# Kernel tuning notes

Measured on AMD Instinct MI355X. Metric: run time of the kernel, lower is better.

The kernel has to match this reference:

```python
import jax, jax.numpy as jnp
import numpy as np
import math

D = 1024      # hidden_size
H = 16        # num_heads
HD = D // H   # head_dim = 64
ROPE = 64     # rope_dim == head_dim (full-head rotation, empty pass-through)
E = 8         # num_experts
F = 2560
BASE = 10000.0
EPS = 1e-5
SPECIALS = jnp.arange(2, 8)  # special_tokens indices {2..7} used as global tokens


def _ln(x, w, b):
    m = x.mean(-1, keepdims=True)
    v = x.var(-1, keepdims=True)  # biased var, matches torch LayerNorm
    return (x - m) / jnp.sqrt(v + EPS) * w + b


def _rope(x, cos, sin):
    # x: [B,H,T,HD]; rotate first ROPE dims via half-split (NOT rotate-half interleave)
    x1, x2 = x[..., : ROPE // 2], x[..., ROPE // 2 : ROPE]
    rot = jnp.concatenate([x1 * cos - x2 * sin, x1 * sin + x2 * cos], axis=-1)
    return jnp.concatenate([rot, x[..., ROPE:]], axis=-1)


def setup_inputs() -> dict:
    key = jax.random.key(0)
    ks = jax.random.split(key, 8)
    B, T = 1, 1024
    g = lambda k, shape, s: (jax.random.normal(k, shape, jnp.float32) * s)
    return {
        "x": g(ks[0], (B, T, D), 1.0),
        "input_ids": jax.random.randint(ks[1], (B, T), 0, 32000),
        "ln1_w": jnp.ones((D,), jnp.float32), "ln1_b": jnp.zeros((D,), jnp.float32),
        "qkv_w": g(ks[2], (D, 3 * D), 0.02), "qkv_b": jnp.zeros((3 * D,), jnp.float32),
        "attn_out_w": g(ks[3], (D, D), 0.02), "attn_out_b": jnp.zeros((D,), jnp.float32),
        "ln2_w": jnp.ones((D,), jnp.float32), "ln2_b": jnp.zeros((D,), jnp.float32),
        "gate_w": g(ks[4], (D, E), 0.02), "gate_b": jnp.zeros((E,), jnp.float32),
        "fc_w": g(ks[5], (E, D, 2 * F), 0.02), "fc_b": jnp.zeros((E, 2 * F), jnp.float32),
        "eout_w": g(ks[6], (E, F, D), 0.02), "eout_b": jnp.zeros((E, D), jnp.float32),
    }


def _block(x, input_ids, ln1_w, ln1_b, qkv_w, qkv_b, attn_out_w, attn_out_b,
           ln2_w, ln2_b, gate_w, gate_b, fc_w, fc_b, eout_w, eout_b):
    B, T, _ = x.shape
    # --- self-attention (pre-norm) ---
    h = _ln(x, ln1_w, ln1_b)
    qkv = h @ qkv_w + qkv_b
    q, k, v = jnp.split(qkv, 3, axis=-1)
    resh = lambda t: t.reshape(B, T, H, HD).transpose(0, 2, 1, 3)  # [B,H,T,HD]
    q, k, v = resh(q), resh(k), resh(v)
    pos = jnp.arange(T, dtype=jnp.float32)
    inv = 1.0 / (BASE ** (jnp.arange(0, ROPE, 2, dtype=jnp.float32) / ROPE))
    fr = pos[:, None] * inv[None, :]            # [T, ROPE/2]
    cos, sin = jnp.cos(fr), jnp.sin(fr)
    q = _rope(q, cos, sin)
    k = _rope(k, cos, sin)
    causal = jnp.tril(jnp.ones((T, T), bool))
    glob = (input_ids[..., None] == SPECIALS).any(-1)            # [B,T]
    allowed = causal[None, None] | glob[:, None, :, None]        # [B,1,T,T]
    logits = jnp.einsum('bhqd,bhkd->bhqk', q, k) / math.sqrt(HD)
    neg = -jnp.finfo(logits.dtype).max
    logits = jnp.where(allowed, logits, neg)
    aw = jax.nn.softmax(logits, axis=-1)
    attn = jnp.einsum('bhqk,bhkd->bhqd', aw, v).transpose(0, 2, 1, 3).reshape(B, T, H * HD)
    x = x + (attn @ attn_out_w + attn_out_b)
    # --- MoE GEGLU FFN (hard top-1 routing) ---
    h2 = _ln(x, ln2_w, ln2_b)
    gp = jax.nn.softmax(h2 @ gate_w + gate_b, axis=-1)           # [B,T,E]
    gw = gp.max(-1)
    gi = gp.argmax(-1)
    xf = h2.reshape(-1, D)
    gif = gi.reshape(-1)
    gwf = gw.reshape(-1)
    N = xf.shape[0]
    outf = jnp.zeros((N, D), x.dtype)
    for e in range(E):  # fixed small expert loop; select by routing mask
        h12 = xf @ fc_w[e] + fc_b[e]
        x1, x2 = h12[:, :F], h12[:, F:]
        y = (x1 * jax.nn.gelu(x2, approximate=False)) @ eout_w[e] + eout_b[e]
        outf = outf + jnp.where((gif == e)[:, None], y, 0.0)
    outf = outf * gwf[:, None]
    sums = jax.ops.segment_sum(gwf, gif, num_segments=E)
    counts = jax.ops.segment_sum(jnp.ones_like(gwf), gif, num_segments=E)
    usage = sums / (counts + 1e-8)
    moe_loss = jnp.sum((usage - 1.0 / E) ** 2)
    return x + outf.reshape(B, T, D), moe_loss


def reference(x, input_ids, ln1_w, ln1_b, qkv_w, qkv_b, attn_out_w, attn_out_b,
              ln2_w, ln2_b, gate_w, gate_b, fc_w, fc_b, eout_w, eout_b):
    return _block(x, input_ids, ln1_w, ln1_b, qkv_w, qkv_b, attn_out_w, attn_out_b,
                  ln2_w, ln2_b, gate_w, gate_b, fc_w, fc_b, eout_w, eout_b)
```

## Files before the change

kernel.cpp:

```cpp
#include <hip/hip_runtime.h>
#include <float.h>
#include <math.h>
#include <stdint.h>

#define T_ 1024
#define D_ 1024
#define H_ 16
#define HD_ 64
#define E_ 8
#define F_ 2560
#define D3_ 3072
#define F2_ 5120

#define WS_H    0u
#define WS_QKV  1048576u
#define WS_ATTN 4194304u
#define WS_X2   5242880u
#define WS_H2   6291456u
#define WS_A    7340032u
#define WS_GW   9961472u
#define WS_GI   9962496u
#define WS_OFFS 9963520u
#define WS_PERM 9963536u

typedef short short8 __attribute__((ext_vector_type(8)));
typedef short short4v __attribute__((ext_vector_type(4)));
typedef __bf16 bf16x8 __attribute__((ext_vector_type(8)));
typedef float floatx4 __attribute__((ext_vector_type(4)));

union FragU { short8 s; bf16x8 b; };

__device__ __forceinline__ short f2bf(float f) {
    union { float f; uint32_t u; } a; a.f = f;
    uint32_t r = a.u + 0x7fffu + ((a.u >> 16) & 1u);
    return (short)(r >> 16);
}

__device__ __forceinline__ void cvt16(const float4& a0, const float4& a1,
                                      const float4& a2, const float4& a3,
                                      short8& c0, short8& c1) {
    c0[0]=f2bf(a0.x); c0[1]=f2bf(a0.y); c0[2]=f2bf(a0.z); c0[3]=f2bf(a0.w);
    c0[4]=f2bf(a1.x); c0[5]=f2bf(a1.y); c0[6]=f2bf(a1.z); c0[7]=f2bf(a1.w);
    c1[0]=f2bf(a2.x); c1[1]=f2bf(a2.y); c1[2]=f2bf(a2.z); c1[3]=f2bf(a2.w);
    c1[4]=f2bf(a3.x); c1[5]=f2bf(a3.y); c1[6]=f2bf(a3.z); c1[7]=f2bf(a3.w);
}

#define GEMM_IDS \
    const int tid  = threadIdx.x;                 \
    const int a_m  = tid >> 1;                    \
    const int a_kh = (tid & 1) * 16;              \
    const int lane = tid & 63, wave = tid >> 6;   \
    const int wm = wave & 1,  wn = wave >> 1;     \
    const int quad = lane >> 4, lm = lane & 15;

__global__ __launch_bounds__(256) void gemm_mfma_full(
    const short* __restrict__ A, int lda,
    const float* __restrict__ B, int ldb,
    const float* __restrict__ bias,
    float* __restrict__ C, int ldc, int K)
{
    __shared__ __align__(16) short As[4*128*8];
    __shared__ __align__(16) short Bs[64*40];
    const int row0 = blockIdx.y * 128, col0 = blockIdx.x * 64;
    GEMM_IDS
    const int b_n = tid >> 2, b_kc = tid & 3;
    floatx4 acc[4][2];
    #pragma unroll
    for (int i=0;i<4;i++)
        #pragma unroll
        for (int j=0;j<2;j++) acc[i][j] = (floatx4){0.f,0.f,0.f,0.f};

    const short* apx = A + (size_t)(row0 + a_m) * lda + a_kh;
    const float* bpx = B + (size_t)(b_kc*8) * ldb + col0 + b_n;
    const int kcA = (tid & 1) * 2;

    short8 sA0, sA1, sB0, sB1;
    float bvA[8], bvB[8];
    sA0 = *(const short8*)(apx);
    sA1 = *(const short8*)(apx + 8);
    sB0 = *(const short8*)(apx + 32);
    sB1 = *(const short8*)(apx + 40);
    #pragma unroll
    for (int j=0;j<8;j++) bvA[j] = bpx[(size_t)j*ldb];
    {
        const float* bp2 = bpx + (size_t)32*ldb;
        #pragma unroll
        for (int j=0;j<8;j++) bvB[j] = bp2[(size_t)j*ldb];
    }

#define GF_STEP(S0,S1,BV,kpre)                                            \
    __syncthreads();                                                      \
    {                                                                     \
        short8 cb;                                                        \
        _Pragma("unroll")                                                 \
        for (int j=0;j<8;j++) cb[j] = f2bf(BV[j]);                        \
        *(short8*)&As[((kcA  )*128 + a_m)*8] = S0;                        \
        *(short8*)&As[((kcA+1)*128 + a_m)*8] = S1;                        \
        *(short8*)&Bs[b_n*40 + b_kc*8] = cb;                              \
    }                                                                     \
    __syncthreads();                                                      \
    if ((kpre) < K) {                                                     \
        S0 = *(const short8*)(apx + (kpre));                              \
        S1 = *(const short8*)(apx + (kpre) + 8);                          \
        const float* bp2 = bpx + (size_t)(kpre) * ldb;                    \
        _Pragma("unroll")                                                 \
        for (int j=0;j<8;j++) BV[j] = bp2[(size_t)j*ldb];                 \
    }                                                                     \
    {                                                                     \
        FragU fa[4], fb[2];                                               \
        _Pragma("unroll")                                                 \
        for (int i=0;i<4;i++) fa[i].s = *(short8*)&As[(quad*128 + wm*64 + i*16 + lm)*8]; \
        _Pragma("unroll")                                                 \
        for (int j=0;j<2;j++) fb[j].s = *(short8*)&Bs[(wn*32 + j*16 + lm)*40 + quad*8];  \
        _Pragma("unroll")                                                 \
        for (int i=0;i<4;i++)                                             \
            _Pragma("unroll")                                             \
            for (int j=0;j<2;j++)                                         \
                acc[i][j] = __builtin_amdgcn_mfma_f32_16x16x32_bf16(fa[i].b, fb[j].b, acc[i][j], 0,0,0); \
    }

    for (int k0 = 0; k0 < K; k0 += 64) {
        GF_STEP(sA0, sA1, bvA, k0 + 64)
        GF_STEP(sB0, sB1, bvB, k0 + 96)
    }
#undef GF_STEP

    #pragma unroll
    for (int i=0;i<4;i++)
        #pragma unroll
        for (int j=0;j<2;j++) {
            int col = col0 + wn*32 + j*16 + lm;
            float bb = bias ? bias[col] : 0.f;
            #pragma unroll
            for (int r=0;r<4;r++) {
                int row = row0 + wm*64 + i*16 + quad*4 + r;
                C[(size_t)row*ldc + col] = acc[i][j][r] + bb;
            }
        }
}

__global__ __launch_bounds__(256) void gemm_mfma_acc(
    const short* __restrict__ A, int lda,
    const float* __restrict__ B, int ldb, long sB,
    const int* __restrict__ offs, const int* __restrict__ perm,
    float* __restrict__ Cacc, int ldc, int K, int nsk)
{
    const int sk = blockIdx.y % nsk;
    const int e  = blockIdx.y / nsk;
    int off = 0, Ne = T_;
    if (offs) { off = offs[e]; Ne = offs[e+1] - off; }
    const int row0 = blockIdx.z * 128;
    if (row0 >= Ne) return;
    const int col0 = blockIdx.x * 64;
    B += (long)e * sB;

    __shared__ __align__(16) short As[4*128*8];
    __shared__ __align__(16) short Bs[64*40];
    __shared__ int toks[128];
    GEMM_IDS
    const int b_n = tid >> 2, b_kc = tid & 3;
    if (tid < 128) {
        int r = row0 + tid;
        toks[tid] = offs ? ((r < Ne) ? perm[off + r] : -1) : r;
    }
    __syncthreads();

    floatx4 acc[4][2];
    #pragma unroll
    for (int i=0;i<4;i++)
        #pragma unroll
        for (int j=0;j<2;j++) acc[i][j] = (floatx4){0.f,0.f,0.f,0.f};

    const int tokA = toks[a_m];
    const short* apx = (tokA >= 0) ? (A + (size_t)tokA * lda + a_kh) : nullptr;
    const float* bpx = B + (size_t)(b_kc*8) * ldb + col0 + b_n;
    const int kcA = (tid & 1) * 2;
    const int Kp = K / nsk;
    const int koff = sk * Kp, kend = koff + Kp;

    short8 sA0 = {0,0,0,0,0,0,0,0}, sA1 = sA0, sB0 = sA0, sB1 = sA0;
    float bvA[8], bvB[8];
    if (apx) {
        sA0 = *(const short8*)(apx + koff);
        sA1 = *(const short8*)(apx + koff + 8);
        sB0 = *(const short8*)(apx + koff + 32);
        sB1 = *(const short8*)(apx + koff + 40);
    }
    {
        const float* bp2 = bpx + (size_t)koff * ldb;
        #pragma unroll
        for (int j=0;j<8;j++) bvA[j] = bp2[(size_t)j*ldb];
        bp2 += (size_t)32 * ldb;
        #pragma unroll
        for (int j=0;j<8;j++) bvB[j] = bp2[(size_t)j*ldb];
    }

#define GA_STEP(S0,S1,BV,kpre)                                            \
    __syncthreads();                                                      \
    {                                                                     \
        short8 cb;                                                        \
        _Pragma("unroll")                                                 \
        for (int j=0;j<8;j++) cb[j] = f2bf(BV[j]);                        \
        *(short8*)&As[((kcA  )*128 + a_m)*8] = S0;                        \
        *(short8*)&As[((kcA+1)*128 + a_m)*8] = S1;                        \
        *(short8*)&Bs[b_n*40 + b_kc*8] = cb;                              \
    }                                                                     \
    __syncthreads();                                                      \
    if ((kpre) < kend) {                                                  \
        if (apx) {                                                        \
            S0 = *(const short8*)(apx + (kpre));                          \
            S1 = *(const short8*)(apx + (kpre) + 8);                      \
        }                                                                 \
        const float* bp2 = bpx + (size_t)(kpre) * ldb;                    \
        _Pragma("unroll")                                                 \
        for (int j=0;j<8;j++) BV[j] = bp2[(size_t)j*ldb];                 \
    }                                                                     \
    {                                                                     \
        FragU fa[4], fb[2];                                               \
        _Pragma("unroll")                                                 \
        for (int i=0;i<4;i++) fa[i].s = *(short8*)&As[(quad*128 + wm*64 + i*16 + lm)*8]; \
        _Pragma("unroll")                                                 \
        for (int j=0;j<2;j++) fb[j].s = *(short8*)&Bs[(wn*32 + j*16 + lm)*40 + quad*8];  \
        _Pragma("unroll")                                                 \
        for (int i=0;i<4;i++)                                             \
            _Pragma("unroll")                                             \
            for (int j=0;j<2;j++)                                         \
                acc[i][j] = __builtin_amdgcn_mfma_f32_16x16x32_bf16(fa[i].b, fb[j].b, acc[i][j], 0,0,0); \
    }

    for (int k0 = koff; k0 < kend; k0 += 64) {
        GA_STEP(sA0, sA1, bvA, k0 + 64)
        GA_STEP(sB0, sB1, bvB, k0 + 96)
    }
#undef GA_STEP

    #pragma unroll
    for (int i=0;i<4;i++)
        #pragma unroll
        for (int j=0;j<2;j++) {
            int col = col0 + wn*32 + j*16 + lm;
            #pragma unroll
            for (int r=0;r<4;r++) {
                int tk = toks[wm*64 + i*16 + quad*4 + r];
                if (tk >= 0) atomicAdd(&Cacc[(size_t)tk*ldc + col], acc[i][j][r]);
            }
        }
}

__global__ __launch_bounds__(256) void moe_fc_mfma(
    const short* __restrict__ h2, const float* __restrict__ fcw,
    const float* __restrict__ fcb, const int* __restrict__ offs,
    const int* __restrict__ perm, short* __restrict__ aout)
{
    const int e = blockIdx.y;
    const int off = offs[e];
    const int Ne = offs[e+1] - off;
    const int row0 = blockIdx.z * 128;
    if (row0 >= Ne) return;
    const int col0 = blockIdx.x * 32;

    __shared__ __align__(16) short As[4*128*8];
    __shared__ __align__(16) short B1s[32*40];
    __shared__ __align__(16) short B2s[32*40];
    __shared__ int toks[128];
    GEMM_IDS
    const int n_l = tid & 31, kg = tid >> 5;
    if (tid < 128) {
        int r = row0 + tid;
        toks[tid] = (r < Ne) ? perm[off + r] : -1;
    }
    __syncthreads();

    floatx4 acc1[4], acc2[4];
    #pragma unroll
    for (int i=0;i<4;i++) {
        acc1[i] = (floatx4){0.f,0.f,0.f,0.f};
        acc2[i] = (floatx4){0.f,0.f,0.f,0.f};
    }

    const float* W = fcw + (size_t)e * D_ * F2_;
    const int tokA = toks[a_m];
    const short* apx = (tokA >= 0) ? (h2 + (size_t)tokA * D_ + a_kh) : nullptr;
    const float* bpx = W + (size_t)(kg*4) * F2_ + col0 + n_l;
    const int kcA = (tid & 1) * 2;

    short8 sA0 = {0,0,0,0,0,0,0,0}, sA1 = sA0, sB0 = sA0, sB1 = sA0;
    float b1A[4], b2A[4], b1B[4], b2B[4];
    if (apx) {
        sA0 = *(const short8*)(apx);
        sA1 = *(const short8*)(apx + 8);
        sB0 = *(const short8*)(apx + 32);
        sB1 = *(const short8*)(apx + 40);
    }
    #pragma unroll
    for (int j=0;j<4;j++) { b1A[j] = bpx[(size_t)j*F2_]; b2A[j] = bpx[(size_t)j*F2_ + F_]; }
    {
        const float* bp2 = bpx + (size_t)32*F2_;
        #pragma unroll
        for (int j=0;j<4;j++) { b1B[j] = bp2[(size_t)j*F2_]; b2B[j] = bp2[(size_t)j*F2_ + F_]; }
    }

#define MF_STEP(S0,S1,BV1,BV2,kpre)                                       \
    __syncthreads();                                                      \
    {                                                                     \
        short4v cb1, cb2;                                                 \
        _Pragma("unroll")                                                 \
        for (int j=0;j<4;j++) { cb1[j] = f2bf(BV1[j]); cb2[j] = f2bf(BV2[j]); } \
        *(short8*)&As[((kcA  )*128 + a_m)*8] = S0;                        \
        *(short8*)&As[((kcA+1)*128 + a_m)*8] = S1;                        \
        *(short4v*)&B1s[n_l*40 + kg*4] = cb1;                             \
        *(short4v*)&B2s[n_l*40 + kg*4] = cb2;                             \
    }                                                                     \
    __syncthreads();                                                      \
    if ((kpre) < D_) {                                                    \
        if (apx) {                                                        \
            S0 = *(const short8*)(apx + (kpre));                          \
            S1 = *(const short8*)(apx + (kpre) + 8);                      \
        }                                                                 \
        const float* bp2 = bpx + (size_t)(kpre) * F2_;                    \
        _Pragma("unroll")                                                 \
        for (int j=0;j<4;j++) { BV1[j] = bp2[(size_t)j*F2_]; BV2[j] = bp2[(size_t)j*F2_ + F_]; } \
    }                                                                     \
    {                                                                     \
        FragU fa[4], fb1, fb2;                                            \
        _Pragma("unroll")                                                 \
        for (int i=0;i<4;i++) fa[i].s = *(short8*)&As[(quad*128 + wm*64 + i*16 + lm)*8]; \
        fb1.s = *(short8*)&B1s[(wn*16 + lm)*40 + quad*8];                 \
        fb2.s = *(short8*)&B2s[(wn*16 + lm)*40 + quad*8];                 \
        _Pragma("unroll")                                                 \
        for (int i=0;i<4;i++) {                                           \
            acc1[i] = __builtin_amdgcn_mfma_f32_16x16x32_bf16(fa[i].b, fb1.b, acc1[i], 0,0,0); \
            acc2[i] = __builtin_amdgcn_mfma_f32_16x16x32_bf16(fa[i].b, fb2.b, acc2[i], 0,0,0); \
        }                                                                 \
    }

    for (int k0 = 0; k0 < D_; k0 += 64) {
        MF_STEP(sA0, sA1, b1A, b2A, k0 + 64)
        MF_STEP(sB0, sB1, b1B, b2B, k0 + 96)
    }
#undef MF_STEP

    {
        int col = col0 + wn*16 + lm;
        float b1 = fcb[(size_t)e*F2_ + col];
        float b2 = fcb[(size_t)e*F2_ + F_ + col];
        #pragma unroll
        for (int i=0;i<4;i++)
            #pragma unroll
            for (int r=0;r<4;r++) {
                int tk = toks[wm*64 + i*16 + quad*4 + r];
                if (tk < 0) continue;
                float v1 = acc1[i][r] + b1;
                float v2 = acc2[i][r] + b2;
                float g = v2 * 0.5f * (1.0f + erff(v2 * 0.70710678118654752f));
                aout[(size_t)tk*F_ + col] = f2bf(v1 * g);
            }
    }
}

__global__ __launch_bounds__(128) void flash_attn(
    const float* __restrict__ qkv, const int* __restrict__ ids,
    short* __restrict__ attnout)
{
    const int h  = blockIdx.y;
    const int q0 = blockIdx.x * 32;
    const int tid = threadIdx.x;
    const int lane = tid & 63, w = tid >> 6;
    const int quad = lane >> 4, lm = lane & 15;

    __shared__ __align__(16) short Qs[32*72];
    __shared__ __align__(16) short Ks[64*72];
    __shared__ __align__(16) short Vt[64*72];
    __shared__ __align__(16) short Ps[2][16*72];
    __shared__ int globf[32];

    {
        int row = tid >> 2, c = (tid & 3) * 16;
        const float* qp = qkv + (size_t)(q0 + row) * D3_ + h * HD_ + c;
        float4 f0 = *(const float4*)(qp);
        float4 f1 = *(const float4*)(qp + 4);
        float4 f2 = *(const float4*)(qp + 8);
        float4 f3 = *(const float4*)(qp + 12);
        short8 s0, s1;
        cvt16(f0, f1, f2, f3, s0, s1);
        *(short8*)&Qs[row*72 + c]     = s0;
        *(short8*)&Qs[row*72 + c + 8] = s1;
    }
    if (tid < 32) {
        int id = ids[q0 + tid];
        globf[tid] = (id >= 2 && id <= 7) ? 1 : 0;
    }
    __syncthreads();

    FragU QA[2];
    #pragma unroll
    for (int s = 0; s < 2; s++)
        QA[s].s = *(short8*)&Qs[(w*16 + lm)*72 + s*32 + quad*8];

    int any = 0;
    #pragma unroll
    for (int i = 0; i < 32; i++) any |= globf[i];
    const int nt = any ? (T_/64) : ((q0 + 31) >> 6) + 1;

    int gq[4]; int qidx[4];
    #pragma unroll
    for (int r = 0; r < 4; r++) {
        int ql = w*16 + quad*4 + r;
        qidx[r] = q0 + ql;
        gq[r] = globf[ql];
    }

    float mrow[4] = {-1e30f, -1e30f, -1e30f, -1e30f};
    float lrow[4] = {0.f, 0.f, 0.f, 0.f};
    floatx4 Oacc[4];
    #pragma unroll
    for (int n = 0; n < 4; n++) Oacc[n] = (floatx4){0.f, 0.f, 0.f, 0.f};

    for (int kt = 0; kt < nt; kt++) {
        __syncthreads();
        #pragma unroll
        for (int rep = 0; rep < 2; rep++) {
            int key = (tid >> 2) + rep*32;
            int c = (tid & 3) * 16;
            const float* kp = qkv + (size_t)(kt*64 + key) * D3_ + D_ + h*HD_ + c;
            float4 f0 = *(const float4*)(kp);
            float4 f1 = *(const float4*)(kp + 4);
            float4 f2 = *(const float4*)(kp + 8);
            float4 f3 = *(const float4*)(kp + 12);
            short8 s0, s1;
            cvt16(f0, f1, f2, f3, s0, s1);
            *(short8*)&Ks[key*72 + c]     = s0;
            *(short8*)&Ks[key*72 + c + 8] = s1;
        }
        #pragma unroll
        for (int rep = 0; rep < 8; rep++) {
            int lin = tid + rep*128;
            int key = lin >> 4;
            int c = (lin & 15) * 4;
            const float* vp = qkv + (size_t)(kt*64 + key) * D3_ + 2*D_ + h*HD_ + c;
            float4 f = *(const float4*)vp;
            Vt[(c+0)*72 + key] = f2bf(f.x);
            Vt[(c+1)*72 + key] = f2bf(f.y);
            Vt[(c+2)*72 + key] = f2bf(f.z);
            Vt[(c+3)*72 + key] = f2bf(f.w);
        }
        __syncthreads();

        floatx4 Sv[4];
        #pragma unroll
        for (int n = 0; n < 4; n++) {
            Sv[n] = (floatx4){0.f, 0.f, 0.f, 0.f};
            #pragma unroll
            for (int s = 0; s < 2; s++) {
                FragU KB;
                KB.s = *(short8*)&Ks[(n*16 + lm)*72 + s*32 + quad*8];
                Sv[n] = __builtin_amdgcn_mfma_f32_16x16x32_bf16(QA[s].b, KB.b, Sv[n], 0, 0, 0);
            }
        }
        #pragma unroll
        for (int n = 0; n < 4; n++) {
            int key = kt*64 + n*16 + lm;
            #pragma unroll
            for (int r = 0; r < 4; r++) {
                float v = Sv[n][r] * 0.125f;
                if (!gq[r] && key > qidx[r]) v = -1e30f;
                Sv[n][r] = v;
            }
        }
        float mnew[4], alpha[4], tsum[4];
        #pragma unroll
        for (int r = 0; r < 4; r++) {
            float tm = fmaxf(fmaxf(Sv[0][r], Sv[1][r]), fmaxf(Sv[2][r], Sv[3][r]));
            #pragma unroll
            for (int x = 1; x < 16; x <<= 1) tm = fmaxf(tm, __shfl_xor(tm, x));
            mnew[r] = fmaxf(mrow[r], tm);
            alpha[r] = __expf(mrow[r] - mnew[r]);
            mrow[r] = mnew[r];
            tsum[r] = 0.f;
        }
        #pragma unroll
        for (int n = 0; n < 4; n++) {
            #pragma unroll
            for (int r = 0; r < 4; r++) {
                float p = __expf(Sv[n][r] - mnew[r]);
                tsum[r] += p;
                Ps[w][(quad*4 + r)*72 + n*16 + lm] = f2bf(p);
            }
        }
        #pragma unroll
        for (int r = 0; r < 4; r++) {
            #pragma unroll
            for (int x = 1; x < 16; x <<= 1) tsum[r] += __shfl_xor(tsum[r], x);
            lrow[r] = lrow[r] * alpha[r] + tsum[r];
        }
        #pragma unroll
        for (int n = 0; n < 4; n++)
            #pragma unroll
            for (int r = 0; r < 4; r++) Oacc[n][r] *= alpha[r];

        #pragma unroll
        for (int s = 0; s < 2; s++) {
            FragU PA;
            PA.s = *(short8*)&Ps[w][lm*72 + s*32 + quad*8];
            #pragma unroll
            for (int n = 0; n < 4; n++) {
                FragU VB;
                VB.s = *(short8*)&Vt[(n*16 + lm)*72 + s*32 + quad*8];
                Oacc[n] = __builtin_amdgcn_mfma_f32_16x16x32_bf16(PA.b, VB.b, Oacc[n], 0, 0, 0);
            }
        }
    }

    #pragma unroll
    for (int n = 0; n < 4; n++)
        #pragma unroll
        for (int r = 0; r < 4; r++) {
            float o = Oacc[n][r] / lrow[r];
            attnout[(size_t)qidx[r]*D_ + h*HD_ + n*16 + lm] = f2bf(o);
        }
}

__global__ __launch_bounds__(256) void ep_attn(
    const float* __restrict__ x, const float* __restrict__ sacc,
    const float* __restrict__ aob, float* __restrict__ x2)
{
    int row = blockIdx.x, tid = threadIdx.x;
    float4 xv = ((const float4*)(x + (size_t)row*D_))[tid];
    float4 sv = ((const float4*)(sacc + (size_t)row*D_))[tid];
    float4 bv = ((const float4*)aob)[tid];
    float4 o;
    o.x = xv.x + sv.x + bv.x; o.y = xv.y + sv.y + bv.y;
    o.z = xv.z + sv.z + bv.z; o.w = xv.w + sv.w + bv.w;
    ((float4*)(x2 + (size_t)row*D_))[tid] = o;
}

__global__ __launch_bounds__(256) void ep_moe(
    const float* __restrict__ x2, const float* __restrict__ sacc,
    const float* __restrict__ eob, const float* __restrict__ gw,
    const int* __restrict__ gi, float* __restrict__ out)
{
    int row = blockIdx.x, tid = threadIdx.x;
    float g = gw[row];
    int e = gi[row];
    float4 xv = ((const float4*)(x2 + (size_t)row*D_))[tid];
    float4 sv = ((const float4*)(sacc + (size_t)row*D_))[tid];
    float4 bv = ((const float4*)(eob + (size_t)e*D_))[tid];
    float4 o;
    o.x = xv.x + g*(sv.x + bv.x); o.y = xv.y + g*(sv.y + bv.y);
    o.z = xv.z + g*(sv.z + bv.z); o.w = xv.w + g*(sv.w + bv.w);
    ((float4*)(out + (size_t)row*D_))[tid] = o;
}

__global__ __launch_bounds__(256) void ln_kernel(
    const float* __restrict__ x, const float* __restrict__ w,
    const float* __restrict__ b, short* __restrict__ out)
{
    const int row = blockIdx.x, tid = threadIdx.x;
    const int lane = tid & 63, wave = tid >> 6;
    float4 v = ((const float4*)(x + (size_t)row * D_))[tid];
    float s  = v.x + v.y + v.z + v.w;
    float sq = v.x*v.x + v.y*v.y + v.z*v.z + v.w*v.w;
    #pragma unroll
    for (int off = 32; off; off >>= 1) {
        s  += __shfl_down(s, off);
        sq += __shfl_down(sq, off);
    }
    __shared__ float rs[4], rq[4], mv[2];
    if (lane == 0) { rs[wave] = s; rq[wave] = sq; }
    __syncthreads();
    if (tid == 0) {
        float ts = rs[0]+rs[1]+rs[2]+rs[3];
        float tq = rq[0]+rq[1]+rq[2]+rq[3];
        float mean = ts * (1.0f / D_);
        float var  = tq * (1.0f / D_) - mean*mean;
        mv[0] = mean; mv[1] = rsqrtf(var + 1e-5f);
    }
    __syncthreads();
    float mean = mv[0], rstd = mv[1];
    float4 wv = ((const float4*)w)[tid];
    float4 bv = ((const float4*)b)[tid];
    short4v o;
    o[0] = f2bf((v.x-mean)*rstd*wv.x + bv.x);
    o[1] = f2bf((v.y-mean)*rstd*wv.y + bv.y);
    o[2] = f2bf((v.z-mean)*rstd*wv.z + bv.z);
    o[3] = f2bf((v.w-mean)*rstd*wv.w + bv.w);
    ((short4v*)(out + (size_t)row * D_))[tid] = o;
}

__global__ __launch_bounds__(256) void rope_kernel(float* __restrict__ qkv)
{
    int gid = blockIdx.x * 256 + threadIdx.x;
    int t = gid >> 9;
    int r = gid & 511;
    int h = r >> 5;
    int d = r & 31;
    float inv = exp2f((float)d * -0.4152410118609203f);
    float fr = (float)t * inv;
    float s, c;
    sincosf(fr, &s, &c);
    float* base = qkv + (size_t)t*D3_ + h*HD_ + d;
    float q1 = base[0], q2 = base[32];
    base[0]  = q1*c - q2*s;
    base[32] = q1*s + q2*c;
    float* kb = base + D_;
    float k1 = kb[0], k2 = kb[32];
    kb[0]  = k1*c - k2*s;
    kb[32] = k1*s + k2*c;
}

__global__ __launch_bounds__(256) void ln2_gate_kernel(
    const float* __restrict__ x2, const float* __restrict__ w,
    const float* __restrict__ b, const float* __restrict__ gwm,
    const float* __restrict__ gbv, short* __restrict__ h2,
    int* __restrict__ gi, float* __restrict__ gw)
{
    const int row = blockIdx.x, tid = threadIdx.x;
    const int lane = tid & 63, wave = tid >> 6;
    float4 v = ((const float4*)(x2 + (size_t)row * D_))[tid];
    float s  = v.x + v.y + v.z + v.w;
    float sq = v.x*v.x + v.y*v.y + v.z*v.z + v.w*v.w;
    #pragma unroll
    for (int off = 32; off; off >>= 1) {
        s  += __shfl_down(s, off);
        sq += __shfl_down(sq, off);
    }
    __shared__ float rs[4], rq[4], mv[2];
    if (lane == 0) { rs[wave] = s; rq[wave] = sq; }
    __syncthreads();
    if (tid == 0) {
        float ts = rs[0]+rs[1]+rs[2]+rs[3];
        float tq = rq[0]+rq[1]+rq[2]+rq[3];
        float mean = ts * (1.0f / D_);
        float var  = tq * (1.0f / D_) - mean*mean;
        mv[0] = mean; mv[1] = rsqrtf(var + 1e-5f);
    }
    __syncthreads();
    float mean = mv[0], rstd = mv[1];
    float4 wv = ((const float4*)w)[tid];
    float4 bv = ((const float4*)b)[tid];
    float hv[4];
    hv[0] = (v.x-mean)*rstd*wv.x + bv.x;
    hv[1] = (v.y-mean)*rstd*wv.y + bv.y;
    hv[2] = (v.z-mean)*rstd*wv.z + bv.z;
    hv[3] = (v.w-mean)*rstd*wv.w + bv.w;
    short4v o;
    o[0]=f2bf(hv[0]); o[1]=f2bf(hv[1]); o[2]=f2bf(hv[2]); o[3]=f2bf(hv[3]);
    ((short4v*)(h2 + (size_t)row * D_))[tid] = o;

    float acc[E_] = {};
    int c = tid * 4;
    #pragma unroll
    for (int j = 0; j < 4; j++) {
        const float* gr = gwm + (size_t)(c+j) * E_;
        #pragma unroll
        for (int e = 0; e < E_; e++) acc[e] += hv[j] * gr[e];
    }
    #pragma unroll
    for (int off = 32; off; off >>= 1)
        #pragma unroll
        for (int e = 0; e < E_; e++) acc[e] += __shfl_down(acc[e], off);
    __shared__ float gred[4][E_];
    if (lane == 0)
        for (int e = 0; e < E_; e++) gred[wave][e] = acc[e];
    __syncthreads();
    if (tid == 0) {
        float lg[E_];
        float mxl = -FLT_MAX; int mi = 0;
        for (int e = 0; e < E_; e++)
            lg[e] = gred[0][e]+gred[1][e]+gred[2][e]+gred[3][e] + gbv[e];
        for (int e = 0; e < E_; e++)
            if (lg[e] > mxl) { mxl = lg[e]; mi = e; }
        float ssum = 0.f;
        for (int e = 0; e < E_; e++) ssum += expf(lg[e] - mxl);
        gi[row] = mi;
        gw[row] = 1.0f / ssum;
    }
}

__global__ void route_kernel(const int* __restrict__ gi,
                             int* __restrict__ offs, int* __restrict__ perm)
{
    __shared__ int cnt[E_], c2[E_], off[E_+1];
    const int tid = threadIdx.x;
    if (tid < E_) { cnt[tid] = 0; c2[tid] = 0; }
    __syncthreads();
    int e = gi[tid];
    atomicAdd(&cnt[e], 1);
    __syncthreads();
    if (tid == 0) {
        off[0] = 0;
        for (int i = 0; i < E_; i++) off[i+1] = off[i] + cnt[i];
        for (int i = 0; i <= E_; i++) offs[i] = off[i];
    }
    __syncthreads();
    int r = atomicAdd(&c2[e], 1);
    perm[off[e] + r] = tid;
}

__global__ void loss_kernel(const int* __restrict__ gi,
                            const float* __restrict__ gw, float* __restrict__ out)
{
    __shared__ float ss[E_], sc[E_];
    const int tid = threadIdx.x;
    if (tid < E_) { ss[tid] = 0.f; sc[tid] = 0.f; }
    __syncthreads();
    for (int t = tid; t < T_; t += 256) {
        int e = gi[t];
        atomicAdd(&ss[e], gw[t]);
        atomicAdd(&sc[e], 1.0f);
    }
    __syncthreads();
    if (tid == 0) {
        float loss = 0.f;
        for (int e = 0; e < E_; e++) {
            float u = ss[e] / (sc[e] + 1e-8f);
            float d = u - 0.125f;
            loss += d * d;
        }
        out[(size_t)T_ * D_] = loss;
    }
}

extern "C" void kernel_launch(void* const* d_in, const int* in_sizes, int n_in,
                              void* d_out, int out_size, void* d_ws, size_t ws_size,
                              hipStream_t stream)
{
    const float* x     = (const float*)d_in[0];
    const int*   ids   = (const int*)d_in[1];
    const float* ln1w  = (const float*)d_in[2];
    const float* ln1b  = (const float*)d_in[3];
    const float* qkvw  = (const float*)d_in[4];
    const float* qkvb  = (const float*)d_in[5];
    const float* aow   = (const float*)d_in[6];
    const float* aob   = (const float*)d_in[7];
    const float* ln2w  = (const float*)d_in[8];
    const float* ln2b  = (const float*)d_in[9];
    const float* gatew = (const float*)d_in[10];
    const float* gateb = (const float*)d_in[11];
    const float* fcw   = (const float*)d_in[12];
    const float* fcb   = (const float*)d_in[13];
    const float* eoutw = (const float*)d_in[14];
    const float* eoutb = (const float*)d_in[15];
    float* out = (float*)d_out;
    float* ws  = (float*)d_ws;

    short* hb    = (short*)(ws + WS_H);
    float* sacc  = ws + WS_H;
    float* qkv   = ws + WS_QKV;
    short* attnb = (short*)(ws + WS_ATTN);
    float* x2    = ws + WS_X2;
    short* h2b   = (short*)(ws + WS_H2);
    short* abuf  = (short*)(ws + WS_A);
    float* gw    = ws + WS_GW;
    int*   gi    = (int*)(ws + WS_GI);
    int*   offs  = (int*)(ws + WS_OFFS);
    int*   perm  = (int*)(ws + WS_PERM);

    ln_kernel<<<T_, 256, 0, stream>>>(x, ln1w, ln1b, hb);
    gemm_mfma_full<<<dim3(D3_/64, T_/128), 256, 0, stream>>>(
        hb, D_, qkvw, D3_, qkvb, qkv, D3_, D_);
    rope_kernel<<<(T_*H_*32)/256, 256, 0, stream>>>(qkv);
    flash_attn<<<dim3(T_/32, H_), 128, 0, stream>>>(qkv, ids, attnb);
    hipMemsetAsync(sacc, 0, (size_t)T_*D_*sizeof(float), stream);
    gemm_mfma_acc<<<dim3(D_/64, 4, T_/128), 256, 0, stream>>>(
        attnb, D_, aow, D_, 0, nullptr, nullptr, sacc, D_, D_, 4);
    ep_attn<<<T_, 256, 0, stream>>>(x, sacc, aob, x2);
    ln2_gate_kernel<<<T_, 256, 0, stream>>>(x2, ln2w, ln2b, gatew, gateb, h2b, gi, gw);
    route_kernel<<<1, T_, 0, stream>>>(gi, offs, perm);
    moe_fc_mfma<<<dim3(F_/32, E_, T_/128), 256, 0, stream>>>(h2b, fcw, fcb, offs, perm, abuf);
    hipMemsetAsync(sacc, 0, (size_t)T_*D_*sizeof(float), stream);
    gemm_mfma_acc<<<dim3(D_/64, 4*E_, T_/128), 256, 0, stream>>>(
        abuf, F_, eoutw, D_, (long)F_*D_, offs, perm, sacc, D_, F_, 4);
    ep_moe<<<T_, 256, 0, stream>>>(x2, sacc, eoutb, gw, gi, out);
    loss_kernel<<<1, 256, 0, stream>>>(gi, gw, out);
}
```

Measured before the change: 548.3 us.

## Split-K the QKV, MoE FC and expert-out GEMMs to raise parallelism

The QKV projection now seeds its output with the bias and runs the atomic split-K GEMM with two K-slices, in place of the full-K kernel. The MoE FC GEMM becomes a two-way split-K kernel that writes raw partial sums to a new workspace buffer, and a separate GLU kernel sums the two partials, adds the bias and applies the erf-GELU gate. The expert-out GEMM split-K goes from 4 to 8. The aim is more blocks to fill the GPU when per-expert row counts are small, at the cost of extra global traffic, atomics, and additional kernel launches.

```diff
diff --git a/kernel.cpp b/kernel.cpp
--- a/kernel.cpp
+++ b/kernel.cpp
@@ -22,6 +22,7 @@
 #define WS_GI   9962496u
 #define WS_OFFS 9963520u
 #define WS_PERM 9963536u
+#define WS_H12  10485760u
 
 typedef short short8 __attribute__((ext_vector_type(8)));
 typedef short short4v __attribute__((ext_vector_type(4)));
@@ -52,92 +53,6 @@
     const int lane = tid & 63, wave = tid >> 6;   \
     const int wm = wave & 1,  wn = wave >> 1;     \
     const int quad = lane >> 4, lm = lane & 15;
-
-__global__ __launch_bounds__(256) void gemm_mfma_full(
-    const short* __restrict__ A, int lda,
-    const float* __restrict__ B, int ldb,
-    const float* __restrict__ bias,
-    float* __restrict__ C, int ldc, int K)
-{
-    __shared__ __align__(16) short As[4*128*8];
-    __shared__ __align__(16) short Bs[64*40];
-    const int row0 = blockIdx.y * 128, col0 = blockIdx.x * 64;
-    GEMM_IDS
-    const int b_n = tid >> 2, b_kc = tid & 3;
-    floatx4 acc[4][2];
-    #pragma unroll
-    for (int i=0;i<4;i++)
-        #pragma unroll
-        for (int j=0;j<2;j++) acc[i][j] = (floatx4){0.f,0.f,0.f,0.f};
-
-    const short* apx = A + (size_t)(row0 + a_m) * lda + a_kh;
-    const float* bpx = B + (size_t)(b_kc*8) * ldb + col0 + b_n;
-    const int kcA = (tid & 1) * 2;
-
-    short8 sA0, sA1, sB0, sB1;
-    float bvA[8], bvB[8];
-    sA0 = *(const short8*)(apx);
-    sA1 = *(const short8*)(apx + 8);
-    sB0 = *(const short8*)(apx + 32);
-    sB1 = *(const short8*)(apx + 40);
-    #pragma unroll
-    for (int j=0;j<8;j++) bvA[j] = bpx[(size_t)j*ldb];
-    {
-        const float* bp2 = bpx + (size_t)32*ldb;
-        #pragma unroll
-        for (int j=0;j<8;j++) bvB[j] = bp2[(size_t)j*ldb];
-    }
-
-#define GF_STEP(S0,S1,BV,kpre)                                            \
-    __syncthreads();                                                      \
-    {                                                                     \
-        short8 cb;                                                        \
-        _Pragma("unroll")                                                 \
-        for (int j=0;j<8;j++) cb[j] = f2bf(BV[j]);                        \
-        *(short8*)&As[((kcA  )*128 + a_m)*8] = S0;                        \
-        *(short8*)&As[((kcA+1)*128 + a_m)*8] = S1;                        \
-        *(short8*)&Bs[b_n*40 + b_kc*8] = cb;                              \
-    }                                                                     \
-    __syncthreads();                                                      \
-    if ((kpre) < K) {                                                     \
-        S0 = *(const short8*)(apx + (kpre));                              \
-        S1 = *(const short8*)(apx + (kpre) + 8);                          \
-        const float* bp2 = bpx + (size_t)(kpre) * ldb;                    \
-        _Pragma("unroll")                                                 \
-        for (int j=0;j<8;j++) BV[j] = bp2[(size_t)j*ldb];                 \
-    }                                                                     \
-    {                                                                     \
-        FragU fa[4], fb[2];                                               \
-        _Pragma("unroll")                                                 \
-        for (int i=0;i<4;i++) fa[i].s = *(short8*)&As[(quad*128 + wm*64 + i*16 + lm)*8]; \
-        _Pragma("unroll")                                                 \
-        for (int j=0;j<2;j++) fb[j].s = *(short8*)&Bs[(wn*32 + j*16 + lm)*40 + quad*8];  \
-        _Pragma("unroll")                                                 \
-        for (int i=0;i<4;i++)                                             \
-            _Pragma("unroll")                                             \
-            for (int j=0;j<2;j++)                                         \
-                acc[i][j] = __builtin_amdgcn_mfma_f32_16x16x32_bf16(fa[i].b, fb[j].b, acc[i][j], 0,0,0); \
-    }
-
-    for (int k0 = 0; k0 < K; k0 += 64) {
-        GF_STEP(sA0, sA1, bvA, k0 + 64)
-        GF_STEP(sB0, sB1, bvB, k0 + 96)
-    }
-#undef GF_STEP
-
-    #pragma unroll
-    for (int i=0;i<4;i++)
-        #pragma unroll
-        for (int j=0;j<2;j++) {
-            int col = col0 + wn*32 + j*16 + lm;
-            float bb = bias ? bias[col] : 0.f;
-            #pragma unroll
-            for (int r=0;r<4;r++) {
-                int row = row0 + wm*64 + i*16 + quad*4 + r;
-                C[(size_t)row*ldc + col] = acc[i][j][r] + bb;
-            }
-        }
-}
 
 __global__ __launch_bounds__(256) void gemm_mfma_acc(
     const short* __restrict__ A, int lda,
@@ -247,114 +162,147 @@
         }
 }
 
-__global__ __launch_bounds__(256) void moe_fc_mfma(
-    const short* __restrict__ h2, const float* __restrict__ fcw,
-    const float* __restrict__ fcb, const int* __restrict__ offs,
-    const int* __restrict__ perm, short* __restrict__ aout)
-{
-    const int e = blockIdx.y;
-    const int off = offs[e];
-    const int Ne = offs[e+1] - off;
+__global__ __launch_bounds__(256) void gemm_fc_sk(
+    const short* __restrict__ A, const float* __restrict__ B,
+    const int* __restrict__ offs, const int* __restrict__ perm,
+    float* __restrict__ Cout)
+{
+    const int sk = blockIdx.y & 1;
+    const int e  = blockIdx.y >> 1;
+    const int off = offs[e], Ne = offs[e+1] - off;
     const int row0 = blockIdx.z * 128;
     if (row0 >= Ne) return;
-    const int col0 = blockIdx.x * 32;
+    const int col0 = blockIdx.x * 64;
+    const float* Bw = B + (size_t)e * D_ * F2_;
 
     __shared__ __align__(16) short As[4*128*8];
-    __shared__ __align__(16) short B1s[32*40];
-    __shared__ __align__(16) short B2s[32*40];
+    __shared__ __align__(16) short Bs[64*40];
     __shared__ int toks[128];
     GEMM_IDS
-    const int n_l = tid & 31, kg = tid >> 5;
+    const int b_n = tid >> 2, b_kc = tid & 3;
     if (tid < 128) {
         int r = row0 + tid;
         toks[tid] = (r < Ne) ? perm[off + r] : -1;
     }
     __syncthreads();
 
-    floatx4 acc1[4], acc2[4];
-    #pragma unroll
-    for (int i=0;i<4;i++) {
-        acc1[i] = (floatx4){0.f,0.f,0.f,0.f};
-        acc2[i] = (floatx4){0.f,0.f,0.f,0.f};
-    }
-
-    const float* W = fcw + (size_t)e * D_ * F2_;
+    floatx4 acc[4][2];
+    #pragma unroll
+    for (int i=0;i<4;i++)
+        #pragma unroll
+        for (int j=0;j<2;j++) acc[i][j] = (floatx4){0.f,0.f,0.f,0.f};
+
     const int tokA = toks[a_m];
-    const short* apx = (tokA >= 0) ? (h2 + (size_t)tokA * D_ + a_kh) : nullptr;
-    const float* bpx = W + (size_t)(kg*4) * F2_ + col0 + n_l;
+    const short* apx = (tokA >= 0) ? (A + (size_t)tokA * D_ + a_kh) : nullptr;
+    const float* bpx = Bw + (size_t)(b_kc*8) * F2_ + col0 + b_n;
     const int kcA = (tid & 1) * 2;
+    const int koff = sk * (D_/2), kend = koff + (D_/2);
 
     short8 sA0 = {0,0,0,0,0,0,0,0}, sA1 = sA0, sB0 = sA0, sB1 = sA0;
-    float b1A[4], b2A[4], b1B[4], b2B[4];
+    float bvA[8], bvB[8];
     if (apx) {
-        sA0 = *(const short8*)(apx);
-        sA1 = *(const short8*)(apx + 8);
-        sB0 = *(const short8*)(apx + 32);
-        sB1 = *(const short8*)(apx + 40);
-    }
-    #pragma unroll
-    for (int j=0;j<4;j++) { b1A[j] = bpx[(size_t)j*F2_]; b2A[j] = bpx[(size_t)j*F2_ + F_]; }
+        sA0 = *(const short8*)(apx + koff);
+        sA1 = *(const short8*)(apx + koff + 8);
+        sB0 = *(const short8*)(apx + koff + 32);
+        sB1 = *(const short8*)(apx + koff + 40);
+    }
     {
-        const float* bp2 = bpx + (size_t)32*F2_;
-        #pragma unroll
-        for (int j=0;j<4;j++) { b1B[j] = bp2[(size_t)j*F2_]; b2B[j] = bp2[(size_t)j*F2_ + F_]; }
-    }
-
-#define MF_STEP(S0,S1,BV1,BV2,kpre)                                       \
+        const float* bp2 = bpx + (size_t)koff * F2_;
+        #pragma unroll
+        for (int j=0;j<8;j++) bvA[j] = bp2[(size_t)j*F2_];
+        bp2 += (size_t)32 * F2_;
+        #pragma unroll
+        for (int j=0;j<8;j++) bvB[j] = bp2[(size_t)j*F2_];
+    }
+
+#define FC_STEP(S0,S1,BV,kpre)                                            \
     __syncthreads();                                                      \
     {                                                                     \
-        short4v cb1, cb2;                                                 \
-        _Pragma("unroll")                                                 \
-        for (int j=0;j<4;j++) { cb1[j] = f2bf(BV1[j]); cb2[j] = f2bf(BV2[j]); } \
+        short8 cb;                                                        \
+        _Pragma("unroll")                                                 \
+        for (int j=0;j<8;j++) cb[j] = f2bf(BV[j]);                        \
         *(short8*)&As[((kcA  )*128 + a_m)*8] = S0;                        \
         *(short8*)&As[((kcA+1)*128 + a_m)*8] = S1;                        \
-        *(short4v*)&B1s[n_l*40 + kg*4] = cb1;                             \
-        *(short4v*)&B2s[n_l*40 + kg*4] = cb2;                             \
+        *(short8*)&Bs[b_n*40 + b_kc*8] = cb;                              \
     }                                                                     \
     __syncthreads();                                                      \
-    if ((kpre) < D_) {                                                    \
+    if ((kpre) < kend) {                                                  \
         if (apx) {                                                        \
             S0 = *(const short8*)(apx + (kpre));                          \
             S1 = *(const short8*)(apx + (kpre) + 8);                      \
         }                                                                 \
         const float* bp2 = bpx + (size_t)(kpre) * F2_;                    \
         _Pragma("unroll")                                                 \
-        for (int j=0;j<4;j++) { BV1[j] = bp2[(size_t)j*F2_]; BV2[j] = bp2[(size_t)j*F2_ + F_]; } \
+        for (int j=0;j<8;j++) BV[j] = bp2[(size_t)j*F2_];                 \
     }                                                                     \
     {                                                                     \
-        FragU fa[4], fb1, fb2;                                            \
+        FragU fa[4], fb[2];                                               \
         _Pragma("unroll")                                                 \
         for (int i=0;i<4;i++) fa[i].s = *(short8*)&As[(quad*128 + wm*64 + i*16 + lm)*8]; \
-        fb1.s = *(short8*)&B1s[(wn*16 + lm)*40 + quad*8];                 \
-        fb2.s = *(short8*)&B2s[(wn*16 + lm)*40 + quad*8];                 \
-        _Pragma("unroll")                                                 \
-        for (int i=0;i<4;i++) {                                           \
-            acc1[i] = __builtin_amdgcn_mfma_f32_16x16x32_bf16(fa[i].b, fb1.b, acc1[i], 0,0,0); \
-            acc2[i] = __builtin_amdgcn_mfma_f32_16x16x32_bf16(fa[i].b, fb2.b, acc2[i], 0,0,0); \
-        }                                                                 \
-    }
-
-    for (int k0 = 0; k0 < D_; k0 += 64) {
-        MF_STEP(sA0, sA1, b1A, b2A, k0 + 64)
-        MF_STEP(sB0, sB1, b1B, b2B, k0 + 96)
-    }
-#undef MF_STEP
-
-    {
-        int col = col0 + wn*16 + lm;
-        float b1 = fcb[(size_t)e*F2_ + col];
-        float b2 = fcb[(size_t)e*F2_ + F_ + col];
-        #pragma unroll
-        for (int i=0;i<4;i++)
+        _Pragma("unroll")                                                 \
+        for (int j=0;j<2;j++) fb[j].s = *(short8*)&Bs[(wn*32 + j*16 + lm)*40 + quad*8];  \
+        _Pragma("unroll")                                                 \
+        for (int i=0;i<4;i++)                                             \
+            _Pragma("unroll")                                             \
+            for (int j=0;j<2;j++)                                         \
+                acc[i][j] = __builtin_amdgcn_mfma_f32_16x16x32_bf16(fa[i].b, fb[j].b, acc[i][j], 0,0,0); \
+    }
+
+    for (int k0 = koff; k0 < kend; k0 += 64) {
+        FC_STEP(sA0, sA1, bvA, k0 + 64)
+        FC_STEP(sB0, sB1, bvB, k0 + 96)
+    }
+#undef FC_STEP
+
+    #pragma unroll
+    for (int i=0;i<4;i++)
+        #pragma unroll
+        for (int j=0;j<2;j++) {
+            int col = col0 + wn*32 + j*16 + lm;
             #pragma unroll
             for (int r=0;r<4;r++) {
                 int tk = toks[wm*64 + i*16 + quad*4 + r];
-                if (tk < 0) continue;
-                float v1 = acc1[i][r] + b1;
-                float v2 = acc2[i][r] + b2;
-                float g = v2 * 0.5f * (1.0f + erff(v2 * 0.70710678118654752f));
-                aout[(size_t)tk*F_ + col] = f2bf(v1 * g);
+                if (tk >= 0)
+                    Cout[((size_t)(sk*T_ + tk))*F2_ + col] = acc[i][j][r];
             }
+        }
+}
+
+__global__ __launch_bounds__(256) void glu_kernel(
+    const float* __restrict__ h12, const float* __restrict__ fcb,
+    const int* __restrict__ gi, short* __restrict__ aout)
+{
+    const int t = blockIdx.x, tid = threadIdx.x;
+    const int e = gi[t];
+    const float* p0 = h12 + (size_t)t * F2_;
+    const float* p1 = h12 + (size_t)(T_ + t) * F2_;
+    const float* fb = fcb + (size_t)e * F2_;
+    for (int c = tid*4; c < F_; c += 1024) {
+        float4 x0 = *(const float4*)(p0 + c);
+        float4 x1 = *(const float4*)(p1 + c);
+        float4 xb = *(const float4*)(fb + c);
+        float4 g0 = *(const float4*)(p0 + F_ + c);
+        float4 g1 = *(const float4*)(p1 + F_ + c);
+        float4 gb = *(const float4*)(fb + F_ + c);
+        float a1[4] = {x0.x+x1.x+xb.x, x0.y+x1.y+xb.y, x0.z+x1.z+xb.z, x0.w+x1.w+xb.w};
+        float a2[4] = {g0.x+g1.x+gb.x, g0.y+g1.y+gb.y, g0.z+g1.z+gb.z, g0.w+g1.w+gb.w};
+        short4v o;
+        #pragma unroll
+        for (int j=0;j<4;j++) {
+            float g = a2[j] * 0.5f * (1.0f + erff(a2[j] * 0.70710678118654752f));
+            o[j] = f2bf(a1[j] * g);
+        }
+        *(short4v*)(aout + (size_t)t*F_ + c) = o;
+    }
+}
+
+__global__ __launch_bounds__(256) void bias_fill(
+    const float* __restrict__ bias, float* __restrict__ buf, int width)
+{
+    const int row = blockIdx.x, tid = threadIdx.x;
+    for (int c = tid*4; c < width; c += 1024) {
+        float4 b = *(const float4*)(bias + c);
+        *(float4*)(buf + (size_t)row*width + c) = b;
     }
 }
 
@@ -755,10 +703,12 @@
     int*   gi    = (int*)(ws + WS_GI);
     int*   offs  = (int*)(ws + WS_OFFS);
     int*   perm  = (int*)(ws + WS_PERM);
+    float* h12   = ws + WS_H12;
 
     ln_kernel<<<T_, 256, 0, stream>>>(x, ln1w, ln1b, hb);
-    gemm_mfma_full<<<dim3(D3_/64, T_/128), 256, 0, stream>>>(
-        hb, D_, qkvw, D3_, qkvb, qkv, D3_, D_);
+    bias_fill<<<T_, 256, 0, stream>>>(qkvb, qkv, D3_);
+    gemm_mfma_acc<<<dim3(D3_/64, 2, T_/128), 256, 0, stream>>>(
+        hb, D_, qkvw, D3_, 0, nullptr, nullptr, qkv, D3_, D_, 2);
     rope_kernel<<<(T_*H_*32)/256, 256, 0, stream>>>(qkv);
     flash_attn<<<dim3(T_/32, H_), 128, 0, stream>>>(qkv, ids, attnb);
     hipMemsetAsync(sacc, 0, (size_t)T_*D_*sizeof(float), stream);
@@ -767,10 +717,11 @@
     ep_attn<<<T_, 256, 0, stream>>>(x, sacc, aob, x2);
     ln2_gate_kernel<<<T_, 256, 0, stream>>>(x2, ln2w, ln2b, gatew, gateb, h2b, gi, gw);
     route_kernel<<<1, T_, 0, stream>>>(gi, offs, perm);
-    moe_fc_mfma<<<dim3(F_/32, E_, T_/128), 256, 0, stream>>>(h2b, fcw, fcb, offs, perm, abuf);
+    gemm_fc_sk<<<dim3(F2_/64, 2*E_, T_/128), 256, 0, stream>>>(h2b, fcw, offs, perm, h12);
+    glu_kernel<<<T_, 256, 0, stream>>>(h12, fcb, gi, abuf);
     hipMemsetAsync(sacc, 0, (size_t)T_*D_*sizeof(float), stream);
-    gemm_mfma_acc<<<dim3(D_/64, 4*E_, T_/128), 256, 0, stream>>>(
-        abuf, F_, eoutw, D_, (long)F_*D_, offs, perm, sacc, D_, F_, 4);
+    gemm_mfma_acc<<<dim3(D_/64, 8*E_, T_/128), 256, 0, stream>>>(
+        abuf, F_, eoutw, D_, (long)F_*D_, offs, perm, sacc, D_, F_, 8);
     ep_moe<<<T_, 256, 0, stream>>>(x2, sacc, eoutb, gw, gi, out);
     loss_kernel<<<1, 256, 0, stream>>>(gi, gw, out);
 }
```

After: 580.8 us. +5.9%, slower.
